# Performance work log

Measured on AMD Instinct MI355X. Metric: run time of the kernel, lower is better.

## Reference

```python
import jax, jax.numpy as jnp
import numpy as np

B, T, C = 4, 2048, 1024
N_HEAD = 16
HEAD_DIM = C // N_HEAD

def setup_inputs() -> dict:
    key = jax.random.key(0)
    k1, k2, k3 = jax.random.split(key, 3)
    x = jax.random.normal(k1, (B, T, C), dtype=jnp.float32)
    # nn.Linear(C, 3C, bias=False): weight [3C, C], y = x @ W.T
    w_qkv = jax.random.normal(k2, (3 * C, C), dtype=jnp.float32) * (1.0 / np.sqrt(C))
    w_proj = jax.random.normal(k3, (C, C), dtype=jnp.float32) * (1.0 / np.sqrt(C))
    return {"x": x, "w_qkv": w_qkv, "w_proj": w_proj}

def reference(x, w_qkv, w_proj):
    Bx, Tx, Cx = x.shape
    qkv = x @ w_qkv.T  # [B,T,3C]
    q, k, v = jnp.split(qkv, 3, axis=-1)
    def heads(t):
        return t.reshape(Bx, Tx, N_HEAD, HEAD_DIM).transpose(0, 2, 1, 3)  # [B,H,T,D]
    q, k, v = heads(q), heads(k), heads(v)
    scale = HEAD_DIM ** -0.5
    att = jnp.einsum('bhtd,bhsd->bhts', q, k) * scale  # [B,H,T,T]
    causal = jnp.tril(jnp.ones((Tx, Tx), dtype=bool))
    att = jnp.where(causal[None, None], att, -jnp.inf)
    att = jax.nn.softmax(att, axis=-1)
    y = jnp.einsum('bhts,bhsd->bhtd', att, v)  # [B,H,T,D]
    y = y.transpose(0, 2, 1, 3).reshape(Bx, Tx, Cx)
    return y @ w_proj.T
```

## Files before the change

kernel.cpp:

```cpp
#include <hip/hip_runtime.h>
#include <hip/hip_bf16.h>

typedef __attribute__((ext_vector_type(8))) short bf16x8;
typedef __attribute__((ext_vector_type(4))) float f32x4;
typedef __attribute__((ext_vector_type(4))) unsigned short ushort4v;
typedef __attribute__((ext_vector_type(2))) unsigned uint2v;

__device__ __forceinline__ unsigned short f2bf(float f) {
  union { float f; unsigned u; } v; v.f = f;
  unsigned r = v.u + 0x7FFFu + ((v.u >> 16) & 1u);
  return (unsigned short)(r >> 16);
}

__device__ __forceinline__ unsigned pack_bf2(float lo, float hi) {
  __hip_bfloat162 h = __float22bfloat162_rn(make_float2(lo, hi));
  union { __hip_bfloat162 h; unsigned u; } cv; cv.h = h; return cv.u;
}

__device__ __forceinline__ void gll16(const void* g, void* l) {
  __builtin_amdgcn_global_load_lds((const __attribute__((address_space(1))) void*)g,
                                   (__attribute__((address_space(3))) void*)l, 16, 0, 0);
}

#define MFMA16(a, b, c) __builtin_amdgcn_mfma_f32_16x16x32_bf16((a), (b), (c), 0, 0, 0)

__global__ void cvt_f32_bf16(const float* __restrict__ s, unsigned short* __restrict__ d, int n) {
  int i = (blockIdx.x * blockDim.x + threadIdx.x) * 4;
  if (i >= n) return;
  float4 f = *(const float4*)(s + i);
  ushort4v r;
  r[0] = f2bf(f.x); r[1] = f2bf(f.y); r[2] = f2bf(f.z); r[3] = f2bf(f.w);
  *(ushort4v*)(d + i) = r;
}

template<int EPI>
__global__ __launch_bounds__(256, 2)
void gemm_nt(const unsigned short* __restrict__ A,
             const unsigned short* __restrict__ B,
             unsigned short* __restrict__ obf,
             float* __restrict__ of32,
             int M, int N, int K) {
  __shared__ unsigned short At[128 * 64];
  __shared__ unsigned short Bt[128 * 64];
  const int tid = threadIdx.x, wid = tid >> 6, lane = tid & 63;
  const int c = lane & 15, g = lane >> 4;
  const int wr = wid >> 1, wc = wid & 1;
  const int m0 = blockIdx.x * 128, n0 = blockIdx.y * 128;

  f32x4 acc[4][4];
#pragma unroll
  for (int i = 0; i < 4; ++i)
#pragma unroll
    for (int j = 0; j < 4; ++j) acc[i][j] = f32x4{0.f, 0.f, 0.f, 0.f};

  for (int kt = 0; kt < K; kt += 64) {
    if (kt) __syncthreads();
#pragma unroll
    for (int r = 0; r < 4; ++r) {
      int chunk = wid * 4 + r;
      int row = chunk * 8 + (lane >> 3);
      int col = (lane & 7) * 8;
      gll16(A + (size_t)(m0 + row) * K + kt + col, At + chunk * 512);
      gll16(B + (size_t)(n0 + row) * K + kt + col, Bt + chunk * 512);
    }
    __syncthreads();
#pragma unroll
    for (int kk = 0; kk < 2; ++kk) {
      bf16x8 af[4], bfr[4];
#pragma unroll
      for (int i = 0; i < 4; ++i) {
        af[i]  = *(const bf16x8*)(At + (wr * 64 + i * 16 + c) * 64 + kk * 32 + g * 8);
        bfr[i] = *(const bf16x8*)(Bt + (wc * 64 + i * 16 + c) * 64 + kk * 32 + g * 8);
      }
#pragma unroll
      for (int mi = 0; mi < 4; ++mi)
#pragma unroll
        for (int ni = 0; ni < 4; ++ni)
          acc[mi][ni] = MFMA16(af[mi], bfr[ni], acc[mi][ni]);
    }
  }

#pragma unroll
  for (int mi = 0; mi < 4; ++mi)
#pragma unroll
    for (int ni = 0; ni < 4; ++ni)
#pragma unroll
      for (int r4 = 0; r4 < 4; ++r4) {
        float v = acc[mi][ni][r4];
        int mg = m0 + wr * 64 + mi * 16 + g * 4 + r4;
        int ng = n0 + wc * 64 + ni * 16 + c;
        if (EPI == 0) {
          int which = ng >> 10, rem = ng & 1023;
          int hh = rem >> 6, dd = rem & 63;
          int bb = mg >> 11, tt = mg & 2047;
          size_t idx = (size_t)which * 8388608u + ((size_t)(bb * 16 + hh) * 2048 + tt) * 64 + dd;
          obf[idx] = f2bf(v);
        } else {
          of32[(size_t)mg * N + ng] = v;
        }
      }
}

__global__ __launch_bounds__(256, 4)
void attn_fwd(const unsigned short* __restrict__ qb,
              const unsigned short* __restrict__ kb,
              const unsigned short* __restrict__ vb,
              unsigned short* __restrict__ yb) {
  __shared__ unsigned short Kt[64 * 64];
  __shared__ unsigned short Vt[64 * 64];
  __shared__ unsigned short Pl[4 * 16 * 72];
  const int tid = threadIdx.x, w = tid >> 6, lane = tid & 63;
  const int c = lane & 15, g = lane >> 4;
  const int bh = blockIdx.x & 63;
  const int qt = 31 - (blockIdx.x >> 6);
  const int q0 = qt * 64;
  const int b = bh >> 4, h = bh & 15;
  const size_t hb = (size_t)bh * 131072;
  const float GAM = 0.125f * 1.44269504089f;

  const unsigned short* qp = qb + hb + (size_t)(q0 + w * 16 + c) * 64;
  bf16x8 qf0 = *(const bf16x8*)(qp + g * 8);
  bf16x8 qf1 = *(const bf16x8*)(qp + 32 + g * 8);

  f32x4 yacc[4];
#pragma unroll
  for (int i = 0; i < 4; ++i) yacc[i] = f32x4{0.f, 0.f, 0.f, 0.f};
  float mrun = -1e30f, lsum = 0.f;
  unsigned short* pw = Pl + w * (16 * 72);

  for (int kv = 0; kv <= qt; ++kv) {
    const int kv0 = kv * 64;
    const bool diag = (kv == qt);
    if (kv) __syncthreads();
#pragma unroll
    for (int r = 0; r < 2; ++r) {
      int chunk = w * 2 + r;
      int row = chunk * 8 + (lane >> 3);
      int bo = (lane & 7) * 16;
      int sbo = bo ^ ((row & 7) << 4);
      gll16((const char*)(kb + hb + (size_t)(kv0 + row) * 64) + sbo, Kt + chunk * 512);
    }
    {
      int kv2 = (lane & 31) * 2;
      int dblk = w * 16 + (lane >> 5) * 8;
      const unsigned short* vp = vb + hb + (size_t)(kv0 + kv2) * 64 + dblk;
      bf16x8 r0 = *(const bf16x8*)(vp);
      bf16x8 r1 = *(const bf16x8*)(vp + 64);
#pragma unroll
      for (int i = 0; i < 8; ++i) {
        int d = dblk + i;
        unsigned pk2 = ((unsigned)(unsigned short)r0[i]) | (((unsigned)(unsigned short)r1[i]) << 16);
        *(unsigned*)(Vt + d * 64 + (kv2 ^ ((d & 7) << 3))) = pk2;
      }
    }
    __syncthreads();

    f32x4 sacc[4];
#pragma unroll
    for (int nt = 0; nt < 4; ++nt) sacc[nt] = f32x4{0.f, 0.f, 0.f, 0.f};
#pragma unroll
    for (int kk = 0; kk < 2; ++kk)
#pragma unroll
      for (int nt = 0; nt < 4; ++nt) {
        int row = nt * 16 + c;
        bf16x8 kf = *(const bf16x8*)(Kt + row * 64 + ((kk * 32 + g * 8) ^ ((row & 7) << 3)));
        sacc[nt] = MFMA16(kf, (kk ? qf1 : qf0), sacc[nt]);
      }

    if (diag) {
      int ql = w * 16 + c;
#pragma unroll
      for (int nt = 0; nt < 4; ++nt)
#pragma unroll
        for (int r = 0; r < 4; ++r)
          if (nt * 16 + g * 4 + r > ql) sacc[nt][r] = -1e30f;
    }

    float m0 = -1e30f;
#pragma unroll
    for (int nt = 0; nt < 4; ++nt) {
      float a = fmaxf(fmaxf(sacc[nt][0], sacc[nt][1]), fmaxf(sacc[nt][2], sacc[nt][3]));
      m0 = fmaxf(m0, a);
    }
    m0 = fmaxf(m0, __shfl_xor(m0, 16));
    m0 = fmaxf(m0, __shfl_xor(m0, 32));

    if (__any(m0 > mrun + 32.0f)) {
      float mnew = fmaxf(mrun, m0);
      float corr = __builtin_amdgcn_exp2f(GAM * (mrun - mnew));
      lsum *= corr;
#pragma unroll
      for (int dt = 0; dt < 4; ++dt) yacc[dt] *= corr;
      mrun = mnew;
    }

    float bexp = -GAM * mrun;
    float psum = 0.f;
#pragma unroll
    for (int nt = 0; nt < 4; ++nt) {
      float p0 = __builtin_amdgcn_exp2f(fmaf(sacc[nt][0], GAM, bexp));
      float p1 = __builtin_amdgcn_exp2f(fmaf(sacc[nt][1], GAM, bexp));
      float p2 = __builtin_amdgcn_exp2f(fmaf(sacc[nt][2], GAM, bexp));
      float p3 = __builtin_amdgcn_exp2f(fmaf(sacc[nt][3], GAM, bexp));
      psum += (p0 + p1) + (p2 + p3);
      uint2v pkv;
      pkv[0] = pack_bf2(p0, p1);
      pkv[1] = pack_bf2(p2, p3);
      *(uint2v*)(pw + c * 72 + nt * 16 + g * 4) = pkv;
    }
    lsum += psum;

#pragma unroll
    for (int kk = 0; kk < 2; ++kk) {
      bf16x8 pb = *(const bf16x8*)(pw + c * 72 + kk * 32 + g * 8);
#pragma unroll
      for (int dt = 0; dt < 4; ++dt) {
        int n = dt * 16 + c;
        bf16x8 vf = *(const bf16x8*)(Vt + n * 64 + ((kk * 32 + g * 8) ^ ((n & 7) << 3)));
        yacc[dt] = MFMA16(vf, pb, yacc[dt]);
      }
    }
  }

  lsum += __shfl_xor(lsum, 16);
  lsum += __shfl_xor(lsum, 32);
  float inv = 1.0f / lsum;
  int row = q0 + w * 16 + c;
  unsigned short* yp = yb + ((size_t)(b * 2048 + row)) * 1024 + h * 64;
#pragma unroll
  for (int dt = 0; dt < 4; ++dt) {
    uint2v pkv;
    pkv[0] = pack_bf2(yacc[dt][0] * inv, yacc[dt][1] * inv);
    pkv[1] = pack_bf2(yacc[dt][2] * inv, yacc[dt][3] * inv);
    *(uint2v*)(yp + dt * 16 + g * 4) = pkv;
  }
}

extern "C" void kernel_launch(void* const* d_in, const int* in_sizes, int n_in,
                              void* d_out, int out_size, void* d_ws, size_t ws_size,
                              hipStream_t stream) {
  const float* x     = (const float*)d_in[0];
  const float* wqkv  = (const float*)d_in[1];
  const float* wproj = (const float*)d_in[2];
  float* out = (float*)d_out;

  unsigned short* ws     = (unsigned short*)d_ws;
  unsigned short* xb     = ws;
  unsigned short* wqkvb  = xb + 8388608;
  unsigned short* wprojb = wqkvb + 3145728;
  unsigned short* qkvb   = wprojb + 1048576;
  unsigned short* yb     = qkvb + 3 * 8388608;

  cvt_f32_bf16<<<8192, 256, 0, stream>>>(x, xb, 8388608);
  cvt_f32_bf16<<<3072, 256, 0, stream>>>(wqkv, wqkvb, 3145728);
  cvt_f32_bf16<<<1024, 256, 0, stream>>>(wproj, wprojb, 1048576);

  gemm_nt<0><<<dim3(64, 24), 256, 0, stream>>>(xb, wqkvb, qkvb, nullptr, 8192, 3072, 1024);
  attn_fwd<<<2048, 256, 0, stream>>>(qkvb, qkvb + 8388608, qkvb + 2 * 8388608, yb);
  gemm_nt<1><<<dim3(64, 8), 256, 0, stream>>>(yb, wprojb, nullptr, out, 8192, 1024, 1024);
}
```

Measured before the change: 180.4 us.

## Rewrite GEMM as 8-wave 256x128 tile with double-buffered swizzled LDS pipeline

```diff
diff --git a/kernel.cpp b/kernel.cpp
--- a/kernel.cpp
+++ b/kernel.cpp
@@ -34,18 +34,42 @@
 }
 
 template<int EPI>
-__global__ __launch_bounds__(256, 2)
-void gemm_nt(const unsigned short* __restrict__ A,
-             const unsigned short* __restrict__ B,
-             unsigned short* __restrict__ obf,
-             float* __restrict__ of32,
-             int M, int N, int K) {
-  __shared__ unsigned short At[128 * 64];
-  __shared__ unsigned short Bt[128 * 64];
+__global__ __launch_bounds__(512, 1)
+void gemm8(const unsigned short* __restrict__ A,
+           const unsigned short* __restrict__ B,
+           unsigned short* __restrict__ obf,
+           float* __restrict__ of32,
+           int M, int N, int K) {
+  extern __shared__ unsigned short lds[];
   const int tid = threadIdx.x, wid = tid >> 6, lane = tid & 63;
   const int c = lane & 15, g = lane >> 4;
   const int wr = wid >> 1, wc = wid & 1;
-  const int m0 = blockIdx.x * 128, n0 = blockIdx.y * 128;
+  const int nbn = N >> 7;
+  const int nwg = gridDim.x;
+  int wg = (blockIdx.x & 7) * (nwg >> 3) + (blockIdx.x >> 3);
+  const int m0 = (wg / nbn) * 256, n0 = (wg % nbn) * 128;
+  const int NT = K >> 6;
+  const size_t rb = (size_t)K * 2;
+  const int swz = (c & 7) << 4;
+
+  const int r8 = lane >> 3;
+  const char* Ag = (const char*)A + (size_t)m0 * rb + (size_t)r8 * rb + (size_t)(((lane & 7) ^ r8) * 16);
+  const char* Bg = (const char*)B + (size_t)n0 * rb + (size_t)r8 * rb + (size_t)(((lane & 7) ^ r8) * 16);
+
+  auto stageA = [&](int t, int par) {
+#pragma unroll
+    for (int j = 0; j < 4; ++j) {
+      int ch = wid * 4 + j;
+      gll16(Ag + (size_t)(ch * 8) * rb + t * 128, lds + par * 16384 + ch * 512);
+    }
+  };
+  auto stageB = [&](int t, int par) {
+#pragma unroll
+    for (int j = 0; j < 2; ++j) {
+      int ch = wid * 2 + j;
+      gll16(Bg + (size_t)(ch * 8) * rb + t * 128, lds + 32768 + par * 8192 + ch * 512);
+    }
+  };
 
   f32x4 acc[4][4];
 #pragma unroll
@@ -53,31 +77,66 @@
 #pragma unroll
     for (int j = 0; j < 4; ++j) acc[i][j] = f32x4{0.f, 0.f, 0.f, 0.f};
 
-  for (int kt = 0; kt < K; kt += 64) {
-    if (kt) __syncthreads();
-#pragma unroll
-    for (int r = 0; r < 4; ++r) {
-      int chunk = wid * 4 + r;
-      int row = chunk * 8 + (lane >> 3);
-      int col = (lane & 7) * 8;
-      gll16(A + (size_t)(m0 + row) * K + kt + col, At + chunk * 512);
-      gll16(B + (size_t)(n0 + row) * K + kt + col, Bt + chunk * 512);
-    }
-    __syncthreads();
-#pragma unroll
-    for (int kk = 0; kk < 2; ++kk) {
-      bf16x8 af[4], bfr[4];
-#pragma unroll
-      for (int i = 0; i < 4; ++i) {
-        af[i]  = *(const bf16x8*)(At + (wr * 64 + i * 16 + c) * 64 + kk * 32 + g * 8);
-        bfr[i] = *(const bf16x8*)(Bt + (wc * 64 + i * 16 + c) * 64 + kk * 32 + g * 8);
-      }
+  stageA(0, 0); stageB(0, 0); stageA(1, 1);
+  asm volatile("s_waitcnt vmcnt(4)" ::: "memory");
+  __builtin_amdgcn_s_barrier();
+
+  for (int t = 0; t < NT; ++t) {
+    const int cur = t & 1;
+    const unsigned short* Ac = lds + cur * 16384;
+    const unsigned short* Bc = lds + 32768 + cur * 8192;
+    bf16x8 af[4][2], bf0[2][2];
+#pragma unroll
+    for (int mi = 0; mi < 4; ++mi) {
+      int arow = wr * 64 + mi * 16 + c;
+#pragma unroll
+      for (int kk = 0; kk < 2; ++kk)
+        af[mi][kk] = *(const bf16x8*)((const char*)Ac + arow * 128 + ((kk * 64 + g * 16) ^ swz));
+    }
+#pragma unroll
+    for (int ni = 0; ni < 2; ++ni) {
+      int brow = wc * 64 + ni * 16 + c;
+#pragma unroll
+      for (int kk = 0; kk < 2; ++kk)
+        bf0[ni][kk] = *(const bf16x8*)((const char*)Bc + brow * 128 + ((kk * 64 + g * 16) ^ swz));
+    }
+    if (t + 1 < NT) stageB(t + 1, cur ^ 1);
+    __builtin_amdgcn_s_barrier();
+    asm volatile("s_waitcnt lgkmcnt(0)" ::: "memory");
+    __builtin_amdgcn_sched_barrier(0);
+    __builtin_amdgcn_s_setprio(1);
+#pragma unroll
+    for (int kk = 0; kk < 2; ++kk)
 #pragma unroll
       for (int mi = 0; mi < 4; ++mi)
 #pragma unroll
-        for (int ni = 0; ni < 4; ++ni)
-          acc[mi][ni] = MFMA16(af[mi], bfr[ni], acc[mi][ni]);
-    }
+        for (int ni = 0; ni < 2; ++ni)
+          acc[mi][ni] = MFMA16(af[mi][kk], bf0[ni][kk], acc[mi][ni]);
+    __builtin_amdgcn_s_setprio(0);
+    __builtin_amdgcn_s_barrier();
+    bf16x8 bf1[2][2];
+#pragma unroll
+    for (int ni = 0; ni < 2; ++ni) {
+      int brow = wc * 64 + (ni + 2) * 16 + c;
+#pragma unroll
+      for (int kk = 0; kk < 2; ++kk)
+        bf1[ni][kk] = *(const bf16x8*)((const char*)Bc + brow * 128 + ((kk * 64 + g * 16) ^ swz));
+    }
+    if (t + 2 < NT) stageA(t + 2, cur);
+    __builtin_amdgcn_s_barrier();
+    asm volatile("s_waitcnt lgkmcnt(0)" ::: "memory");
+    __builtin_amdgcn_sched_barrier(0);
+    __builtin_amdgcn_s_setprio(1);
+#pragma unroll
+    for (int kk = 0; kk < 2; ++kk)
+#pragma unroll
+      for (int mi = 0; mi < 4; ++mi)
+#pragma unroll
+        for (int ni = 0; ni < 2; ++ni)
+          acc[mi][ni + 2] = MFMA16(af[mi][kk], bf1[ni][kk], acc[mi][ni + 2]);
+    __builtin_amdgcn_s_setprio(0);
+    asm volatile("s_waitcnt vmcnt(4)" ::: "memory");
+    __builtin_amdgcn_s_barrier();
   }
 
 #pragma unroll
@@ -255,7 +314,7 @@
   cvt_f32_bf16<<<3072, 256, 0, stream>>>(wqkv, wqkvb, 3145728);
   cvt_f32_bf16<<<1024, 256, 0, stream>>>(wproj, wprojb, 1048576);
 
-  gemm_nt<0><<<dim3(64, 24), 256, 0, stream>>>(xb, wqkvb, qkvb, nullptr, 8192, 3072, 1024);
+  gemm8<0><<<768, 512, 98304, stream>>>(xb, wqkvb, qkvb, nullptr, 8192, 3072, 1024);
   attn_fwd<<<2048, 256, 0, stream>>>(qkvb, qkvb + 8388608, qkvb + 2 * 8388608, yb);
-  gemm_nt<1><<<dim3(64, 8), 256, 0, stream>>>(yb, wprojb, nullptr, out, 8192, 1024, 1024);
-}
+  gemm8<1><<<256, 512, 98304, stream>>>(yb, wprojb, nullptr, out, 8192, 1024, 1024);
+}
```

Measured after the change: 175.3 us. 2.9% less time.

## Replace GEMM with 256x256 8-wave double-buffered pipelined kernel

Applied to the files above, without the earlier changes.

```diff
diff --git a/kernel.cpp b/kernel.cpp
--- a/kernel.cpp
+++ b/kernel.cpp
@@ -34,61 +34,125 @@
 }
 
 template<int EPI>
-__global__ __launch_bounds__(256, 2)
-void gemm_nt(const unsigned short* __restrict__ A,
-             const unsigned short* __restrict__ B,
-             unsigned short* __restrict__ obf,
-             float* __restrict__ of32,
-             int M, int N, int K) {
-  __shared__ unsigned short At[128 * 64];
-  __shared__ unsigned short Bt[128 * 64];
+__global__ __launch_bounds__(512, 1)
+void gemm8p(const unsigned short* __restrict__ A,
+            const unsigned short* __restrict__ B,
+            unsigned short* __restrict__ obf,
+            float* __restrict__ of32,
+            int M, int N, int K) {
+  extern __shared__ char lds[];
   const int tid = threadIdx.x, wid = tid >> 6, lane = tid & 63;
   const int c = lane & 15, g = lane >> 4;
-  const int wr = wid >> 1, wc = wid & 1;
-  const int m0 = blockIdx.x * 128, n0 = blockIdx.y * 128;
-
-  f32x4 acc[4][4];
-#pragma unroll
-  for (int i = 0; i < 4; ++i)
+  const int wm = wid >> 2, wn = wid & 3;
+  const int nbn = N >> 8;
+  const int nwg = gridDim.x;
+  const int wg = (blockIdx.x & 7) * (nwg >> 3) + (blockIdx.x >> 3);
+  const int m0 = (wg / nbn) * 256, n0 = (wg % nbn) * 256;
+  const int NT = K >> 6, NT2 = NT >> 1;
+  const size_t rb = (size_t)K * 2;
+  const int sw = (c & 7) << 4;
+
+  const int srow = tid >> 3;
+  const int sslot = (tid & 7) ^ (srow & 7);
+  const char* Ag = (const char*)A + (size_t)(m0 + srow) * rb + sslot * 16;
+  const char* Bg = (const char*)B + (size_t)(n0 + srow) * rb + sslot * 16;
+  char* ldsw = lds + wid * 1024;
+
+  auto stg = [&](const char* G, int obase, int t, int h) {
+#pragma unroll
+    for (int j = 0; j < 2; ++j)
+      gll16(G + (size_t)(h * 128 + j * 64) * rb + t * 128,
+            ldsw + obase + (t & 1) * 32768 + h * 16384 + j * 8192);
+  };
+
+  f32x4 acc[8][4];
+#pragma unroll
+  for (int i = 0; i < 8; ++i)
 #pragma unroll
     for (int j = 0; j < 4; ++j) acc[i][j] = f32x4{0.f, 0.f, 0.f, 0.f};
 
-  for (int kt = 0; kt < K; kt += 64) {
-    if (kt) __syncthreads();
-#pragma unroll
-    for (int r = 0; r < 4; ++r) {
-      int chunk = wid * 4 + r;
-      int row = chunk * 8 + (lane >> 3);
-      int col = (lane & 7) * 8;
-      gll16(A + (size_t)(m0 + row) * K + kt + col, At + chunk * 512);
-      gll16(B + (size_t)(n0 + row) * K + kt + col, Bt + chunk * 512);
-    }
-    __syncthreads();
-#pragma unroll
-    for (int kk = 0; kk < 2; ++kk) {
-      bf16x8 af[4], bfr[4];
-#pragma unroll
-      for (int i = 0; i < 4; ++i) {
-        af[i]  = *(const bf16x8*)(At + (wr * 64 + i * 16 + c) * 64 + kk * 32 + g * 8);
-        bfr[i] = *(const bf16x8*)(Bt + (wc * 64 + i * 16 + c) * 64 + kk * 32 + g * 8);
-      }
+  bf16x8 afA[4][2], afB[4][2], bl[2][2], bh[2][2];
+
+  auto rdA = [&](int par, int s, bf16x8 af[4][2]) {
+    const char* base = lds + par * 32768 + wm * 16384;
+#pragma unroll
+    for (int mi = 0; mi < 4; ++mi) {
+      int lr = s * 64 + mi * 16 + c;
+#pragma unroll
+      for (int kk = 0; kk < 2; ++kk)
+        af[mi][kk] = *(const bf16x8*)(base + lr * 128 + ((kk * 64 + g * 16) ^ sw));
+    }
+  };
+  auto rdB = [&](int par, int s, bf16x8 bf[2][2]) {
+    const char* base = lds + 65536 + par * 32768 + (wn >> 1) * 16384;
+#pragma unroll
+    for (int ni = 0; ni < 2; ++ni) {
+      int lr = (wn & 1) * 64 + s * 32 + ni * 16 + c;
+#pragma unroll
+      for (int kk = 0; kk < 2; ++kk)
+        bf[ni][kk] = *(const bf16x8*)(base + lr * 128 + ((kk * 64 + g * 16) ^ sw));
+    }
+  };
+  auto mma = [&](bf16x8 af[4][2], bf16x8 bf[2][2], int sm, int sn) {
+    asm volatile("s_waitcnt lgkmcnt(0)" ::: "memory");
+    __builtin_amdgcn_sched_barrier(0);
+    __builtin_amdgcn_s_setprio(1);
+#pragma unroll
+    for (int kk = 0; kk < 2; ++kk)
 #pragma unroll
       for (int mi = 0; mi < 4; ++mi)
 #pragma unroll
-        for (int ni = 0; ni < 4; ++ni)
-          acc[mi][ni] = MFMA16(af[mi], bfr[ni], acc[mi][ni]);
-    }
+        for (int ni = 0; ni < 2; ++ni)
+          acc[sm * 4 + mi][sn * 2 + ni] = MFMA16(af[mi][kk], bf[ni][kk], acc[sm * 4 + mi][sn * 2 + ni]);
+    __builtin_amdgcn_s_setprio(0);
+  };
+
+  auto halfIter = [&](int par, int tA, bool vA, int tB, bool vB, bool drainAll) {
+    rdA(par, 0, afA); rdB(par, 0, bl);
+    if (vA) stg(Ag, 0, tA, 0);
+    __builtin_amdgcn_s_barrier();
+    mma(afA, bl, 0, 0);
+    __builtin_amdgcn_s_barrier();
+    rdB(par, 1, bh);
+    if (vA) stg(Ag, 0, tA, 1);
+    __builtin_amdgcn_s_barrier();
+    mma(afA, bh, 0, 1);
+    __builtin_amdgcn_s_barrier();
+    rdA(par, 1, afB);
+    if (vB) stg(Bg, 65536, tB, 0);
+    __builtin_amdgcn_s_barrier();
+    mma(afB, bh, 1, 1);
+    __builtin_amdgcn_s_barrier();
+    if (vB) stg(Bg, 65536, tB, 1);
+    __builtin_amdgcn_s_barrier();
+    mma(afB, bl, 1, 0);
+    if (drainAll) { asm volatile("s_waitcnt vmcnt(0)" ::: "memory"); }
+    else          { asm volatile("s_waitcnt vmcnt(4)" ::: "memory"); }
+    __builtin_amdgcn_s_barrier();
+  };
+
+  stg(Bg, 65536, 0, 0); stg(Bg, 65536, 0, 1);
+  stg(Ag, 0, 0, 0);     stg(Ag, 0, 0, 1);
+  stg(Bg, 65536, 1, 0); stg(Bg, 65536, 1, 1);
+  asm volatile("s_waitcnt vmcnt(4)" ::: "memory");
+  __builtin_amdgcn_s_barrier();
+
+  for (int i = 0; i < NT2; ++i) {
+    const int u = 2 * i;
+    const bool last = (i == NT2 - 1);
+    halfIter(0, u + 1, true,  u + 2, !last, last);
+    halfIter(1, u + 2, !last, u + 3, !last, last);
   }
 
 #pragma unroll
-  for (int mi = 0; mi < 4; ++mi)
+  for (int mi = 0; mi < 8; ++mi)
 #pragma unroll
     for (int ni = 0; ni < 4; ++ni)
 #pragma unroll
       for (int r4 = 0; r4 < 4; ++r4) {
         float v = acc[mi][ni][r4];
-        int mg = m0 + wr * 64 + mi * 16 + g * 4 + r4;
-        int ng = n0 + wc * 64 + ni * 16 + c;
+        int mg = m0 + wm * 128 + mi * 16 + g * 4 + r4;
+        int ng = n0 + wn * 64 + ni * 16 + c;
         if (EPI == 0) {
           int which = ng >> 10, rem = ng & 1023;
           int hh = rem >> 6, dd = rem & 63;
@@ -101,7 +165,7 @@
       }
 }
 
-__global__ __launch_bounds__(256, 4)
+__global__ __launch_bounds__(256, 6)
 void attn_fwd(const unsigned short* __restrict__ qb,
               const unsigned short* __restrict__ kb,
               const unsigned short* __restrict__ vb,
@@ -255,7 +319,7 @@
   cvt_f32_bf16<<<3072, 256, 0, stream>>>(wqkv, wqkvb, 3145728);
   cvt_f32_bf16<<<1024, 256, 0, stream>>>(wproj, wprojb, 1048576);
 
-  gemm_nt<0><<<dim3(64, 24), 256, 0, stream>>>(xb, wqkvb, qkvb, nullptr, 8192, 3072, 1024);
+  gemm8p<0><<<384, 512, 131072, stream>>>(xb, wqkvb, qkvb, nullptr, 8192, 3072, 1024);
   attn_fwd<<<2048, 256, 0, stream>>>(qkvb, qkvb + 8388608, qkvb + 2 * 8388608, yb);
-  gemm_nt<1><<<dim3(64, 8), 256, 0, stream>>>(yb, wprojb, nullptr, out, 8192, 1024, 1024);
-}
+  gemm8p<1><<<128, 512, 131072, stream>>>(yb, wprojb, nullptr, out, 8192, 1024, 1024);
+}
```

New measurement: 176.0 us. 2.5% less time.
